# Performance work log

Hardware: AMD Instinct MI355X
Metric: run time of the kernel (lower is better)

The kernel has to match this reference:

```python
import jax, jax.numpy as jnp
import numpy as np

N_NODES, N_EDGES = 8000, 24000
MUL0_IN, MUL1_IN = 64, 32          # node: 64x0e + 32x1o
MUL0_MSG, MUL1_MSG = 16, 32        # msg:  16x0e + 32x1o
GATE_S, N_GATES = 16, 32           # gate scalars / gates (= mul of 32x1o gated)
RADIAL = 128
EDGE_DIM = 4                       # 1x0e + 1x1o
WNUM = MUL0_IN*MUL0_MSG + MUL0_IN*MUL1_MSG + MUL1_IN*MUL1_MSG + MUL1_IN*MUL0_MSG  # 4608
INV_SQRT3 = 1.0 / np.sqrt(3.0)     # wigner-3j(1,1,0)/(0,1,1)/(1,0,1) magnitude
# e3nn path weights: sqrt(ir_out.dim / sum_paths_into_output(num_elements))
PW_MSG0 = np.sqrt(1.0 / (MUL0_IN + MUL1_IN))                   # tp_msg -> 16x0e
PW_MSG1 = np.sqrt(3.0 / (MUL0_IN + MUL1_IN))                   # tp_msg -> 32x1o
PW_G01 = np.sqrt(1.0 / (MUL0_MSG*MUL0_IN + MUL1_MSG*MUL1_IN))  # FCTP -> 0e outs
PW_G2  = np.sqrt(3.0 / (MUL0_MSG*MUL1_IN + MUL1_MSG*MUL0_IN))  # FCTP -> 1o out
PW_H0 = np.sqrt(1.0 / (GATE_S + MUL1_MSG*MUL1_MSG))            # heavy_tp -> 16x0e
PW_H1 = np.sqrt(3.0 / (GATE_S + GATE_S))                       # heavy_tp -> 32x1o

_trapz = getattr(np, 'trapezoid', np.trapz)
def _cst(f):
    # e3nn normalize2mom constant: 1/sqrt(E_{z~N(0,1)}[f(z)^2])
    xs = np.linspace(-12.0, 12.0, 200001)
    pdf = np.exp(-0.5*xs*xs) / np.sqrt(2.0*np.pi)
    return float(1.0 / np.sqrt(_trapz(f(xs)**2 * pdf, xs)))
CST_SILU = _cst(lambda v: v / (1.0 + np.exp(-v)))
CST_SIG  = _cst(lambda v: 1.0 / (1.0 + np.exp(-v)))
CST_TANH = _cst(np.tanh)


def setup_inputs() -> dict:
    key = jax.random.key(0)
    ks = jax.random.split(key, 19)
    f = lambda k, s: jax.random.normal(k, s, dtype=jnp.float32)
    x = f(ks[0], (N_NODES, MUL0_IN + 3*MUL1_IN))
    edge_attr = f(ks[1], (N_EDGES, EDGE_DIM))
    edge_index = jax.random.randint(ks[2], (2, N_EDGES), 0, N_NODES)
    z = jax.random.randint(ks[3], (N_NODES,), 0, 10)
    canonical = jax.random.randint(ks[4], (N_NODES,), 0, N_NODES)
    W_mlp1 = f(ks[5], (EDGE_DIM, RADIAL))
    W_mlp2 = f(ks[6], (RADIAL, WNUM))
    Wg000 = f(ks[7], (MUL0_MSG, MUL0_IN, GATE_S))
    Wg110 = f(ks[8], (MUL1_MSG, MUL1_IN, GATE_S))
    Wg001 = f(ks[9], (MUL0_MSG, MUL0_IN, N_GATES))
    Wg111 = f(ks[10], (MUL1_MSG, MUL1_IN, N_GATES))
    Wg012 = f(ks[11], (MUL0_MSG, MUL1_IN, MUL1_MSG))
    Wg102 = f(ks[12], (MUL1_MSG, MUL0_IN, MUL1_MSG))
    Wa = f(ks[13], (GATE_S, GATE_S))
    Wb = f(ks[14], (GATE_S, MUL1_MSG))
    Wc = f(ks[15], (MUL1_MSG, GATE_S))
    Wd = f(ks[16], (MUL1_MSG, MUL1_MSG, GATE_S))
    WL0 = f(ks[17], (GATE_S, GATE_S))
    WL1 = f(ks[18], (MUL1_MSG, MUL1_MSG))
    return dict(x=x, edge_attr=edge_attr, W_mlp1=W_mlp1, W_mlp2=W_mlp2,
                Wg000=Wg000, Wg110=Wg110, Wg001=Wg001, Wg111=Wg111,
                Wg012=Wg012, Wg102=Wg102, Wa=Wa, Wb=Wb, Wc=Wc, Wd=Wd,
                WL0=WL0, WL1=WL1, edge_index=edge_index, z=z, canonical=canonical)


def _forward(x, edge_attr, W_mlp1, W_mlp2, Wg000, Wg110, Wg001, Wg111,
             Wg012, Wg102, Wa, Wb, Wc, Wd, WL0, WL1, edge_index, z, canonical):
    N = x.shape[0]
    E = edge_attr.shape[0]
    src, dst = edge_index[0], edge_index[1]
    # ---- radial MLP -> per-edge TP weights (e3nn FullyConnectedNet, normalized silu)
    h = CST_SILU * jax.nn.silu(edge_attr @ (W_mlp1 / np.sqrt(float(EDGE_DIM))))
    w = h @ (W_mlp2 / np.sqrt(float(RADIAL)))                 # (E, 4608)
    s000 = w[:, 0:1024].reshape(E, MUL0_IN, MUL0_MSG)
    s011 = w[:, 1024:3072].reshape(E, MUL0_IN, MUL1_MSG)
    s101 = w[:, 3072:4096].reshape(E, MUL1_IN, MUL1_MSG)
    s110 = w[:, 4096:4608].reshape(E, MUL1_IN, MUL0_MSG)
    # ---- gather source nodes, per-edge equivariant tensor product
    xs0 = x[src, :MUL0_IN]                                    # (E,64)
    xs1 = x[src, MUL0_IN:].reshape(E, MUL1_IN, 3)             # (E,32,3)
    a0 = edge_attr[:, 0]
    a1 = edge_attr[:, 1:4]
    msg0 = PW_MSG0 * (jnp.einsum('e,eu,euw->ew', a0, xs0, s000)
                      + INV_SQRT3 * jnp.einsum('eum,em,euw->ew', xs1, a1, s110))
    msg1 = PW_MSG1 * INV_SQRT3 * (jnp.einsum('eu,em,euw->ewm', xs0, a1, s011)
                                  + jnp.einsum('eum,e,euw->ewm', xs1, a0, s101))
    msg = jnp.concatenate([msg0, msg1.reshape(E, -1)], axis=-1)   # (E,112)
    # ---- scatter_add to destination nodes
    nm = jax.ops.segment_sum(msg, dst, num_segments=N)
    m0 = nm[:, :MUL0_MSG]
    m1 = nm[:, MUL0_MSG:].reshape(N, MUL1_MSG, 3)
    x0 = x[:, :MUL0_IN]
    x1 = x[:, MUL0_IN:].reshape(N, MUL1_IN, 3)
    # ---- FullyConnectedTensorProduct(msg, node) -> scalars | gates | gated
    gs = PW_G01 * (jnp.einsum('nu,nv,uvw->nw', m0, x0, Wg000)
                   + INV_SQRT3 * jnp.einsum('num,nvm,uvw->nw', m1, x1, Wg110))
    gg = PW_G01 * (jnp.einsum('nu,nv,uvw->nw', m0, x0, Wg001)
                   + INV_SQRT3 * jnp.einsum('num,nvm,uvw->nw', m1, x1, Wg111))
    gv = PW_G2 * INV_SQRT3 * (jnp.einsum('nu,nvm,uvw->nwm', m0, x1, Wg012)
                              + jnp.einsum('num,nv,uvw->nwm', m1, x0, Wg102))
    # ---- Gate (normalized sigmoid / tanh)
    xg0 = CST_SIG * jax.nn.sigmoid(gs)                        # (N,16)
    gates = CST_TANH * jnp.tanh(gg)                           # (N,32)
    xg1 = gates[:, :, None] * gv                              # (N,32,3)
    xg = jnp.concatenate([xg0, xg1.reshape(N, -1)], axis=-1)  # (N,112)
    # ---- heavy-atom pooling: scatter_mean of heavy nodes by canonical id
    mask = z > 1
    mf = mask.astype(x.dtype)
    sums = jax.ops.segment_sum(xg * mf[:, None], canonical, num_segments=N)
    cnt = jax.ops.segment_sum(mf, canonical, num_segments=N)
    xh = sums / jnp.maximum(cnt, 1.0)[:, None]
    h0 = xh[:, :GATE_S]
    h1 = xh[:, GATE_S:].reshape(N, MUL1_MSG, 3)
    # ---- heavy self tensor product (internal shared weights)
    t0 = PW_H0 * (jnp.einsum('uv,nu,nv->nu', Wa, h0, h0)
                  + INV_SQRT3 * jnp.einsum('uvw,num,nvm->nw', Wd, h1, h1))
    t1 = PW_H1 * INV_SQRT3 * (jnp.einsum('uv,nu,nvm->nvm', Wb, h0, h1)
                              + jnp.einsum('uv,num,nv->num', Wc, h1, h0))
    th = jnp.concatenate([t0, t1.reshape(N, -1)], axis=-1)
    # ---- broadcast heavy features back to heavy atoms
    y = jnp.where(mask[:, None], th[canonical], xg)
    y0 = y[:, :GATE_S]
    y1 = y[:, GATE_S:].reshape(N, MUL1_MSG, 3)
    # ---- e3nn Linear (per-irrep, 1/sqrt(fan_in))
    out0 = y0 @ (WL0 / np.sqrt(float(GATE_S)))
    out1 = jnp.einsum('num,uw->nwm', y1, WL1) / np.sqrt(float(MUL1_MSG))
    return jnp.concatenate([out0, out1.reshape(N, -1)], axis=-1)  # (N,112)


def reference(x, edge_attr, W_mlp1, W_mlp2, Wg000, Wg110, Wg001, Wg111,
              Wg012, Wg102, Wa, Wb, Wc, Wd, WL0, WL1, edge_index, z, canonical):
    return _forward(x, edge_attr, W_mlp1, W_mlp2, Wg000, Wg110, Wg001, Wg111,
                    Wg012, Wg102, Wa, Wb, Wc, Wd, WL0, WL1, edge_index, z, canonical)
```

## Files before the change

### kernel.cpp

```cpp
#include <hip/hip_runtime.h>
#include <hip/hip_bf16.h>
#include <cmath>


#define N_NODES 8000
#define N_EDGES 24000

#define INV_SQRT3f 0.57735026918962576f
#define PW_MSG0f 0.10206207261596575f
#define PW1f     0.10206207261596575f
#define PW_G01f  0.022097086912079608f
#define PW_G2f   0.034232659844072866f
#define PW_H0f   0.031008683647302115f
#define PW_H1f   0.30618621784789724f
#define RSQRT128f 0.08838834764831845f
#define RSQRT32f  0.17677669529663687f

typedef short short8 __attribute__((ext_vector_type(8)));
typedef short short4v __attribute__((ext_vector_type(4)));
typedef float f32x4 __attribute__((ext_vector_type(4)));

__device__ inline short f32_to_bf16_bits(float v) {
  unsigned int b = __builtin_bit_cast(unsigned int, v);
  b += 0x7fffu + ((b >> 16) & 1u);
  return (short)(b >> 16);
}

__global__ __launch_bounds__(256) void k1_h(const float* __restrict__ ea,
                                            const float* __restrict__ W1,
                                            short* __restrict__ hbf,
                                            float cst_silu) {
  int idx = blockIdx.x * 256 + threadIdx.x;
  int e = idx >> 5, q = idx & 31;
  const float a0 = ea[e*4+0], a1 = ea[e*4+1], a2 = ea[e*4+2], a3 = ea[e*4+3];
  const float4 w0 = *(const float4*)&W1[q*4];
  const float4 w1 = *(const float4*)&W1[128 + q*4];
  const float4 w2 = *(const float4*)&W1[256 + q*4];
  const float4 w3 = *(const float4*)&W1[384 + q*4];
  float s[4] = {0.5f*(a0*w0.x + a1*w1.x + a2*w2.x + a3*w3.x),
                0.5f*(a0*w0.y + a1*w1.y + a2*w2.y + a3*w3.y),
                0.5f*(a0*w0.z + a1*w1.z + a2*w2.z + a3*w3.z),
                0.5f*(a0*w0.w + a1*w1.w + a2*w2.w + a3*w3.w)};
  short4v o;
#pragma unroll
  for (int i = 0; i < 4; ++i) {
    float sg = 1.f / (1.f + expf(-s[i]));
    o[i] = f32_to_bf16_bits(cst_silu * s[i] * sg * RSQRT128f);
  }
  *(short4v*)&hbf[idx*4] = o;
}

__global__ __launch_bounds__(256) void k_prep(const float* __restrict__ W2,
                                              const float* __restrict__ Wg000,
                                              const float* __restrict__ Wg110,
                                              const float* __restrict__ Wg001,
                                              const float* __restrict__ Wg111,
                                              const float* __restrict__ Wg012,
                                              const float* __restrict__ Wg102,
                                              const float* __restrict__ Wd,
                                              const float* __restrict__ WL0,
                                              const float* __restrict__ WL1,
                                              short* __restrict__ w2s,
                                              short* __restrict__ bt,
                                              float* __restrict__ wdt,
                                              float* __restrict__ wl0t,
                                              float* __restrict__ wl1t) {
  const int b = blockIdx.x, tid = threadIdx.x;
  if (b < 576) {
    __shared__ float tile[32][33];
    const int kt = b & 3, ct = b >> 2;
    const int k0 = kt*32, c0 = ct*32;
    const int tx = tid & 31, ty = tid >> 5;
#pragma unroll
    for (int i = 0; i < 4; ++i) {
      int r = ty + i*8;
      tile[r][tx] = W2[(k0+r)*4608 + c0 + tx];
    }
    __syncthreads();
#pragma unroll
    for (int i = 0; i < 4; ++i) {
      int r = ty + i*8;
      const int c = c0 + r, k = k0 + tx;
      const int id = (c < 1024) ? (c >> 4)
                   : (c < 4096) ? ((c + 512) >> 4) : ((c - 3072) >> 4);
      const int nn = c & 15, ks = k >> 5, quad = (k >> 3) & 3, jj = k & 7;
      w2s[id*2048 + ks*512 + (quad*16 + nn)*8 + jj] = f32_to_bf16_bits(tile[tx][r]);
    }
  } else if (b < 1344) {
    int i = (b - 576) * 256 + tid;
    float v;
    if (i < 16384) {
      int u = i >> 10, r = i & 1023;
      int ks = r >> 9, lane = (r >> 3) & 63, j = r & 7;
      int k = ks*32 + (lane >> 4)*8 + j, nn = lane & 15;
      v = Wg000[u*1024 + k*16 + nn];
    } else if (i < 49152) {
      int o = i - 16384;
      int tau = o >> 10, r = o & 1023;
      int u = tau >> 1, wh = tau & 1;
      int ks = r >> 9, lane = (r >> 3) & 63, j = r & 7;
      int k = ks*32 + (lane >> 4)*8 + j, nn = lane & 15;
      v = Wg001[u*2048 + k*32 + wh*16 + nn];
    } else if (i < 65536) {
      int o = i - 49152;
      int u = o >> 9, r = o & 511;
      int lane = r >> 3, j = r & 7;
      int k = (lane >> 4)*8 + j, nn = lane & 15;
      v = INV_SQRT3f * Wg110[u*512 + k*16 + nn];
    } else if (i < 98304) {
      int o = i - 65536;
      int tau = o >> 9, r = o & 511;
      int u = tau >> 1, wh = tau & 1;
      int lane = r >> 3, j = r & 7;
      int k = (lane >> 4)*8 + j, nn = lane & 15;
      v = INV_SQRT3f * Wg111[u*1024 + k*32 + wh*16 + nn];
    } else if (i < 131072) {
      int o = i - 98304;
      int tau = o >> 9, r = o & 511;
      int vv = tau >> 1, wh = tau & 1;
      int lane = r >> 3, j = r & 7;
      int k = (lane >> 4)*8 + j, nn = lane & 15;
      v = (k < 16) ? Wg012[k*1024 + vv*32 + wh*16 + nn] : 0.f;
    } else {
      int o = i - 131072;
      int tau = o >> 10, r = o & 1023;
      int u = tau >> 1, wh = tau & 1;
      int ks = r >> 9, lane = (r >> 3) & 63, j = r & 7;
      int k = ks*32 + (lane >> 4)*8 + j, nn = lane & 15;
      v = Wg102[u*2048 + k*32 + wh*16 + nn];
    }
    bt[i] = f32_to_bf16_bits(v);
  } else {
    int i = (b - 1344) * 256 + tid;
    if (i < 16384) {
      int k = i >> 10, uv = i & 1023;
      wdt[i] = Wd[uv*16 + k];
    } else if (i < 16640) {
      int j = i - 16384; int jj = j >> 4, v = j & 15;
      wl0t[j] = WL0[v*16 + jj];
    } else if (i < 17664) {
      int j = i - 16640; int w = j >> 5, u = j & 31;
      wl1t[j] = WL1[u*32 + w];
    }
  }
}

__global__ __launch_bounds__(256, 2) void k2_edge_msg(
    const float* __restrict__ x, const float* __restrict__ ea,
    const short* __restrict__ w2s, const short* __restrict__ hbf,
    const int* __restrict__ ei, float* __restrict__ nm) {
  __shared__ float msg_s[32][116];
  __shared__ float x0pt[64][32];
  __shared__ float z2wt[32][32];
  __shared__ float x1wt[32][32][3];
  __shared__ float a_s[32][4];
  __shared__ int srcs_s[32], dsts_s[32];

  const int tid = threadIdx.x;
  const int e0 = blockIdx.x * 32;

  if (tid < 32) { srcs_s[tid] = ei[e0+tid]; dsts_s[tid] = ei[N_EDGES + e0 + tid]; }
  if (tid < 128) a_s[tid>>2][tid&3] = ea[e0*4 + tid];
  for (int i = tid; i < 32*116; i += 256) (&msg_s[0][0])[i] = 0.f;
  __syncthreads();

  for (int i = tid; i < 2048; i += 256) {
    int e = i >> 6, u = i & 63;
    x0pt[u][e] = PW1f * x[srcs_s[e]*160 + u];
  }
  for (int i = tid; i < 1024; i += 256) {
    int e = i >> 5, u = i & 31;
    const float* xp = &x[srcs_s[e]*160 + 64 + u*3];
    float m0v = xp[0], m1v = xp[1], m2v = xp[2];
    float a0 = a_s[e][0];
    z2wt[u][e] = PW_MSG0f * INV_SQRT3f *
                 (m0v*a_s[e][1] + m1v*a_s[e][2] + m2v*a_s[e][3]);
    x1wt[u][e][0] = PW1f * a0 * m0v;
    x1wt[u][e][1] = PW1f * a0 * m1v;
    x1wt[u][e][2] = PW1f * a0 * m2v;
  }
  __syncthreads();

  const int lane = tid & 63, wv = tid >> 6;
  const int quad = lane >> 4, nn = lane & 15;
  const int eq = quad * 4;

  short8 af[2][4];
#pragma unroll
  for (int t = 0; t < 2; ++t)
#pragma unroll
    for (int ks = 0; ks < 4; ++ks)
      af[t][ks] = *(const short8*)&hbf[(e0 + t*16 + nn)*128 + ks*32 + quad*8];

  float p000[2][4] = {};
  float p0[2][4] = {};
  float p011[2][4] = {};
  float p101[2][4][3] = {};

  short8 B0[4], B1[4], B2[4];
  auto loadB = [&](short8* B, int id) {
    const int idc = (id < 287) ? id : 287;
    const short* p = w2s + idc*2048 + lane*8;
    B[0] = *(const short8*)(p);
    B[1] = *(const short8*)(p + 512);
    B[2] = *(const short8*)(p + 1024);
    B[3] = *(const short8*)(p + 1536);
  };
  auto process = [&](const short8* B, int id) {
    f32x4 c0 = {0.f,0.f,0.f,0.f}, c1 = {0.f,0.f,0.f,0.f};
    c0 = __builtin_amdgcn_mfma_f32_16x16x32_bf16(af[0][0], B[0], c0, 0,0,0);
    c1 = __builtin_amdgcn_mfma_f32_16x16x32_bf16(af[1][0], B[0], c1, 0,0,0);
    c0 = __builtin_amdgcn_mfma_f32_16x16x32_bf16(af[0][1], B[1], c0, 0,0,0);
    c1 = __builtin_amdgcn_mfma_f32_16x16x32_bf16(af[1][1], B[1], c1, 0,0,0);
    c0 = __builtin_amdgcn_mfma_f32_16x16x32_bf16(af[0][2], B[2], c0, 0,0,0);
    c1 = __builtin_amdgcn_mfma_f32_16x16x32_bf16(af[1][2], B[2], c1, 0,0,0);
    c0 = __builtin_amdgcn_mfma_f32_16x16x32_bf16(af[0][3], B[3], c0, 0,0,0);
    c1 = __builtin_amdgcn_mfma_f32_16x16x32_bf16(af[1][3], B[3], c1, 0,0,0);
    if (id < 64) {
      const f32x4 w0 = *(const f32x4*)&x0pt[id][eq];
      const f32x4 w1 = *(const f32x4*)&x0pt[id][16 + eq];
#pragma unroll
      for (int r = 0; r < 4; ++r) { p000[0][r] += w0[r]*c0[r]; p000[1][r] += w1[r]*c1[r]; }
    } else if (id < 96) {
      const int u = id - 64;
      const f32x4 w0 = *(const f32x4*)&z2wt[u][eq];
      const f32x4 w1 = *(const f32x4*)&z2wt[u][16 + eq];
#pragma unroll
      for (int r = 0; r < 4; ++r) { p0[0][r] += w0[r]*c0[r]; p0[1][r] += w1[r]*c1[r]; }
    } else if (id < 224) {
      const int u = (id - 96) >> 1;
      const f32x4 w0 = *(const f32x4*)&x0pt[u][eq];
      const f32x4 w1 = *(const f32x4*)&x0pt[u][16 + eq];
#pragma unroll
      for (int r = 0; r < 4; ++r) { p011[0][r] += w0[r]*c0[r]; p011[1][r] += w1[r]*c1[r]; }
    } else {
      const int u = (id - 224) >> 1;
#pragma unroll
      for (int r = 0; r < 4; ++r) {
        const float* xw0 = &x1wt[u][eq + r][0];
        const float* xw1 = &x1wt[u][16 + eq + r][0];
        p101[0][r][0] += xw0[0]*c0[r]; p101[0][r][1] += xw0[1]*c0[r]; p101[0][r][2] += xw0[2]*c0[r];
        p101[1][r][0] += xw1[0]*c1[r]; p101[1][r][1] += xw1[1]*c1[r]; p101[1][r][2] += xw1[2]*c1[r];
      }
    }
  };

  loadB(B0, wv); loadB(B1, wv + 4);
  int id = wv;
  for (int j = 0; j < 24; ++j) {
    loadB(B2, id + 8);  __builtin_amdgcn_sched_barrier(0); process(B0, id);
    loadB(B0, id + 12); __builtin_amdgcn_sched_barrier(0); process(B1, id + 4);
    loadB(B1, id + 16); __builtin_amdgcn_sched_barrier(0); process(B2, id + 8);
    id += 12;
  }

  const int wcol = (wv & 1)*16 + nn;
#pragma unroll
  for (int t = 0; t < 2; ++t)
#pragma unroll
    for (int r = 0; r < 4; ++r) {
      const int e = t*16 + eq + r;
      atomicAdd(&msg_s[e][nn], a_s[e][0]*p000[t][r] + p0[t][r]);
      const float q = p011[t][r];
      atomicAdd(&msg_s[e][16 + wcol*3 + 0], a_s[e][1]*q + p101[t][r][0]);
      atomicAdd(&msg_s[e][16 + wcol*3 + 1], a_s[e][2]*q + p101[t][r][1]);
      atomicAdd(&msg_s[e][16 + wcol*3 + 2], a_s[e][3]*q + p101[t][r][2]);
    }
  __syncthreads();

  for (int i = tid; i < 32*112; i += 256) {
    int le = i / 112, slot = i - le*112;
    atomicAdd(&nm[dsts_s[le]*112 + slot], msg_s[le][slot]);
  }
}

__global__ __launch_bounds__(256, 2) void k3_gate(const float* __restrict__ x,
                                                  const float* __restrict__ nm,
                                                  const short* __restrict__ bt,
                                                  const int* __restrict__ z,
                                                  const int* __restrict__ canonical,
                                                  float* __restrict__ xg,
                                                  float* __restrict__ sums,
                                                  float* __restrict__ cnt,
                                                  float cst_sig, float cst_tanh) {
  __shared__ short x0b[16][64];
  __shared__ short x1b[3][16][32];
  __shared__ short m0b[16][32];
  __shared__ float m0t[16][16];
  __shared__ float m1t[32][3][16];
  __shared__ float x1t[32][3][16];
  __shared__ float gs_s[16][20];
  __shared__ float gg_s[16][36];
  __shared__ float gv_s[16][100];
  const int tid = threadIdx.x;
  const int n0 = blockIdx.x * 16;

  for (int i = tid; i < 16*160; i += 256) {
    int n = i / 160, f = i - n*160;
    float v = x[(n0+n)*160 + f];
    if (f < 64) x0b[n][f] = f32_to_bf16_bits(v);
    else {
      int j = f - 64; int vv = j/3, m = j - vv*3;
      x1b[m][n][vv] = f32_to_bf16_bits(v);
      x1t[vv][m][n] = v;
    }
  }
  for (int i = tid; i < 16*112; i += 256) {
    int n = i / 112, f = i - n*112;
    float v = nm[(n0+n)*112 + f];
    if (f < 16) { m0b[n][f] = f32_to_bf16_bits(v); m0t[f][n] = v; }
    else { int j = f - 16; int u = j/3, m = j - u*3; m1t[u][m][n] = v; }
  }
  { int n = tid >> 4, k = tid & 15; m0b[n][16+k] = 0; }
  for (int i = tid; i < 320; i += 256) (&gs_s[0][0])[i] = 0.f;
  for (int i = tid; i < 576; i += 256) (&gg_s[0][0])[i] = 0.f;
  for (int i = tid; i < 1600; i += 256) (&gv_s[0][0])[i] = 0.f;
  __syncthreads();

  const int lane = tid & 63, wv = tid >> 6;
  const int quad = lane >> 4, nn = lane & 15;
  const int eq = quad * 4;
  const int wh = wv & 1, uw = wv >> 1;
  const int l8 = lane * 8;

  const short8 ax0a = *(const short8*)&x0b[nn][quad*8];
  const short8 ax0c = *(const short8*)&x0b[nn][32 + quad*8];
  short8 ax1[3];
#pragma unroll
  for (int m = 0; m < 3; ++m) ax1[m] = *(const short8*)&x1b[m][nn][quad*8];
  const short8 am0 = *(const short8*)&m0b[nn][quad*8];

  const short* b000 = bt;
  const short* b001 = bt + 16384;
  const short* b110 = bt + 49152;
  const short* b111 = bt + 65536;
  const short* b012 = bt + 98304;
  const short* b102 = bt + 131072;

  float gs_p[4] = {}, gg_p[4] = {};
  float gv_p[3][4] = {};

  {
    int u = wv;
    const short* p = b000 + u*1024 + l8;
    short8 ba = *(const short8*)p, bb = *(const short8*)(p + 512);
    for (int i = 0; i < 4; ++i) {
      const int un = (i < 3) ? u + 4 : u;
      const short* np = b000 + un*1024 + l8;
      short8 na = *(const short8*)np, nb = *(const short8*)(np + 512);
      __builtin_amdgcn_sched_barrier(0);
      f32x4 c = {0.f,0.f,0.f,0.f};
      c = __builtin_amdgcn_mfma_f32_16x16x32_bf16(ax0a, ba, c, 0,0,0);
      c = __builtin_amdgcn_mfma_f32_16x16x32_bf16(ax0c, bb, c, 0,0,0);
      const f32x4 t = *(const f32x4*)&m0t[u][eq];
#pragma unroll
      for (int r = 0; r < 4; ++r) gs_p[r] += t[r]*c[r];
      u = un; ba = na; bb = nb;
    }
  }
  {
    int u = wv;
    short8 s0 = *(const short8*)(b110 + u*512 + l8);
    for (int i = 0; i < 8; ++i) {
      const int un = (i < 7) ? u + 4 : u;
      short8 ns = *(const short8*)(b110 + un*512 + l8);
      __builtin_amdgcn_sched_barrier(0);
      f32x4 c0 = {0.f,0.f,0.f,0.f}, c1 = {0.f,0.f,0.f,0.f}, c2 = {0.f,0.f,0.f,0.f};
      c0 = __builtin_amdgcn_mfma_f32_16x16x32_bf16(ax1[0], s0, c0, 0,0,0);
      c1 = __builtin_amdgcn_mfma_f32_16x16x32_bf16(ax1[1], s0, c1, 0,0,0);
      c2 = __builtin_amdgcn_mfma_f32_16x16x32_bf16(ax1[2], s0, c2, 0,0,0);
      const f32x4 t0 = *(const f32x4*)&m1t[u][0][eq];
      const f32x4 t1 = *(const f32x4*)&m1t[u][1][eq];
      const f32x4 t2 = *(const f32x4*)&m1t[u][2][eq];
#pragma unroll
      for (int r = 0; r < 4; ++r) gs_p[r] += t0[r]*c0[r] + t1[r]*c1[r] + t2[r]*c2[r];
      u = un; s0 = ns;
    }
  }
  {
    int u = uw;
    const short* p = b001 + (u*2 + wh)*1024 + l8;
    short8 ba = *(const short8*)p, bb = *(const short8*)(p + 512);
    for (int j = 0; j < 8; ++j) {
      const int un = (j < 7) ? u + 2 : u;
      const short* np = b001 + (un*2 + wh)*1024 + l8;
      short8 na = *(const short8*)np, nb = *(const short8*)(np + 512);
      __builtin_amdgcn_sched_barrier(0);
      f32x4 c = {0.f,0.f,0.f,0.f};
      c = __builtin_amdgcn_mfma_f32_16x16x32_bf16(ax0a, ba, c, 0,0,0);
      c = __builtin_amdgcn_mfma_f32_16x16x32_bf16(ax0c, bb, c, 0,0,0);
      const f32x4 t = *(const f32x4*)&m0t[u][eq];
#pragma unroll
      for (int r = 0; r < 4; ++r) gg_p[r] += t[r]*c[r];
      u = un; ba = na; bb = nb;
    }
  }
  {
    int u = uw;
    short8 s0 = *(const short8*)(b111 + (u*2 + wh)*512 + l8);
    for (int j = 0; j < 16; ++j) {
      const int un = (j < 15) ? u + 2 : u;
      short8 ns = *(const short8*)(b111 + (un*2 + wh)*512 + l8);
      __builtin_amdgcn_sched_barrier(0);
      f32x4 c0 = {0.f,0.f,0.f,0.f}, c1 = {0.f,0.f,0.f,0.f}, c2 = {0.f,0.f,0.f,0.f};
      c0 = __builtin_amdgcn_mfma_f32_16x16x32_bf16(ax1[0], s0, c0, 0,0,0);
      c1 = __builtin_amdgcn_mfma_f32_16x16x32_bf16(ax1[1], s0, c1, 0,0,0);
      c2 = __builtin_amdgcn_mfma_f32_16x16x32_bf16(ax1[2], s0, c2, 0,0,0);
      const f32x4 t0 = *(const f32x4*)&m1t[u][0][eq];
      const f32x4 t1 = *(const f32x4*)&m1t[u][1][eq];
      const f32x4 t2 = *(const f32x4*)&m1t[u][2][eq];
#pragma unroll
      for (int r = 0; r < 4; ++r) gg_p[r] += t0[r]*c0[r] + t1[r]*c1[r] + t2[r]*c2[r];
      u = un; s0 = ns;
    }
  }
  {
    int v = uw;
    short8 s0 = *(const short8*)(b012 + (v*2 + wh)*512 + l8);
    for (int j = 0; j < 16; ++j) {
      const int vn = (j < 15) ? v + 2 : v;
      short8 ns = *(const short8*)(b012 + (vn*2 + wh)*512 + l8);
      __builtin_amdgcn_sched_barrier(0);
      f32x4 c = {0.f,0.f,0.f,0.f};
      c = __builtin_amdgcn_mfma_f32_16x16x32_bf16(am0, s0, c, 0,0,0);
#pragma unroll
      for (int m = 0; m < 3; ++m) {
        const f32x4 t = *(const f32x4*)&x1t[v][m][eq];
#pragma unroll
        for (int r = 0; r < 4; ++r) gv_p[m][r] += t[r]*c[r];
      }
      v = vn; s0 = ns;
    }
  }
  {
    int u = uw;
    const short* p = b102 + (u*2 + wh)*1024 + l8;
    short8 ba = *(const short8*)p, bb = *(const short8*)(p + 512);
    for (int j = 0; j < 16; ++j) {
      const int un = (j < 15) ? u + 2 : u;
      const short* np = b102 + (un*2 + wh)*1024 + l8;
      short8 na = *(const short8*)np, nb = *(const short8*)(np + 512);
      __builtin_amdgcn_sched_barrier(0);
      f32x4 c = {0.f,0.f,0.f,0.f};
      c = __builtin_amdgcn_mfma_f32_16x16x32_bf16(ax0a, ba, c, 0,0,0);
      c = __builtin_amdgcn_mfma_f32_16x16x32_bf16(ax0c, bb, c, 0,0,0);
#pragma unroll
      for (int m = 0; m < 3; ++m) {
        const f32x4 t = *(const f32x4*)&m1t[u][m][eq];
#pragma unroll
        for (int r = 0; r < 4; ++r) gv_p[m][r] += t[r]*c[r];
      }
      u = un; ba = na; bb = nb;
    }
  }

#pragma unroll
  for (int r = 0; r < 4; ++r) {
    atomicAdd(&gs_s[eq + r][nn], gs_p[r]);
    atomicAdd(&gg_s[eq + r][wh*16 + nn], gg_p[r]);
#pragma unroll
    for (int m = 0; m < 3; ++m)
      atomicAdd(&gv_s[eq + r][(wh*16 + nn)*3 + m], gv_p[m][r]);
  }
  __syncthreads();

  for (int i = tid; i < 16*112; i += 256) {
    int n = i / 112, f = i - n*112;
    float o;
    if (f < 16) {
      o = cst_sig / (1.f + expf(-PW_G01f * gs_s[n][f]));
    } else {
      int j = f - 16; int w = j/3;
      float gate = cst_tanh * tanhf(PW_G01f * gg_s[n][w]);
      o = gate * (PW_G2f * INV_SQRT3f) * gv_s[n][j];
    }
    const int gn = n0 + n;
    xg[gn*112 + f] = o;
    if (z[gn] > 1) {
      const int c = canonical[gn];
      atomicAdd(&sums[c*112 + f], o);
      if (f == 0) atomicAdd(&cnt[c], 1.f);
    }
  }
}

__global__ __launch_bounds__(256) void k5_thead(const float* __restrict__ sums,
                                                const float* __restrict__ cnt,
                                                const float* __restrict__ Wa,
                                                const float* __restrict__ Wb,
                                                const float* __restrict__ Wc,
                                                const float* __restrict__ wdt,
                                                float* __restrict__ th) {
  __shared__ float xh_s[8][112];
  __shared__ float cm_s[8][1024];
  __shared__ float red[256];
  const int tid = threadIdx.x;
  const int n0 = blockIdx.x * 8;
  for (int i = tid; i < 8*112; i += 256) {
    int n = i / 112, j = i - n*112;
    float cv = fmaxf(cnt[n0+n], 1.f);
    xh_s[n][j] = sums[(n0+n)*112 + j] / cv;
  }
  __syncthreads();
  for (int i = tid; i < 8192; i += 256) {
    int n = i >> 10, uv = i & 1023, u = uv >> 5, v = uv & 31;
    const float* hh = xh_s[n] + 16;
    cm_s[n][uv] = hh[u*3]*hh[v*3] + hh[u*3+1]*hh[v*3+1] + hh[u*3+2]*hh[v*3+2];
  }
  __syncthreads();
  {
    const int hs = tid >> 7, p = tid & 127;
    const int n = p >> 4, k = p & 15;
    float wd = 0.f;
    const float* cp = cm_s[n] + hs*512;
    const float* wp = wdt + k*1024 + hs*512;
#pragma unroll 4
    for (int uv = 0; uv < 512; uv += 4) {
      const f32x4 a = *(const f32x4*)&cp[uv];
      const f32x4 bq = *(const f32x4*)&wp[uv];
      wd += a[0]*bq[0] + a[1]*bq[1] + a[2]*bq[2] + a[3]*bq[3];
    }
    red[tid] = wd;
  }
  __syncthreads();
  if (tid < 128) {
    int n = tid >> 4, k = tid & 15;
    float sA = 0.f;
    for (int v = 0; v < 16; ++v) sA += Wa[k*16+v]*xh_s[n][v];
    float wd = red[tid] + red[tid + 128];
    th[(n0+n)*112 + k] = PW_H0f*(xh_s[n][k]*sA + INV_SQRT3f*wd);
  }
  {
    int n = tid >> 5, j = tid & 31;
    float wb = 0.f, wc = 0.f;
    for (int u = 0; u < 16; ++u) wb += Wb[u*32+j]*xh_s[n][u];
    for (int v = 0; v < 16; ++v) wc += Wc[j*16+v]*xh_s[n][v];
    float cb = PW_H1f * INV_SQRT3f * (wb + wc);
    const float* hh = xh_s[n] + 16;
    float* o = th + (n0+n)*112 + 16 + j*3;
    o[0] = cb*hh[j*3]; o[1] = cb*hh[j*3+1]; o[2] = cb*hh[j*3+2];
  }
}

__global__ __launch_bounds__(256) void k6_out(const float* __restrict__ xg,
                                              const float* __restrict__ th,
                                              const int* __restrict__ z,
                                              const int* __restrict__ canonical,
                                              const float* __restrict__ wl0t,
                                              const float* __restrict__ wl1t,
                                              float* __restrict__ out) {
  int idx = blockIdx.x * 256 + threadIdx.x;
  int n = idx / 112, j = idx - n*112;
  const float* yr = (z[n] > 1) ? (th + canonical[n]*112) : (xg + n*112);
  float o = 0.f;
  if (j < 16) {
    const float* wp = wl0t + j*16;
#pragma unroll 4
    for (int v = 0; v < 16; ++v) o += yr[v]*wp[v];
    o *= 0.25f;
  } else {
    int jj = j - 16, w = jj / 3, m = jj - w*3;
    const float* wp = wl1t + w*32;
#pragma unroll 4
    for (int u = 0; u < 32; ++u) o += yr[16 + u*3 + m]*wp[u];
    o *= RSQRT32f;
  }
  out[idx] = o;
}

namespace {
struct Csts {
  float silu, sig, tanh_;
  Csts() {
    const int NPT = 200001;
    const double a = -12.0, b = 12.0;
    const double dx = (b - a) / (NPT - 1);
    double s1 = 0.0, s2 = 0.0, s3 = 0.0;
    for (int i = 0; i < NPT; ++i) {
      double xv = a + dx*i;
      double pdf = std::exp(-0.5*xv*xv) / std::sqrt(2.0*M_PI);
      double sg = 1.0 / (1.0 + std::exp(-xv));
      double f1 = xv*sg, f2 = sg, f3 = std::tanh(xv);
      double wg = (i == 0 || i == NPT-1) ? 0.5 : 1.0;
      s1 += wg*f1*f1*pdf; s2 += wg*f2*f2*pdf; s3 += wg*f3*f3*pdf;
    }
    silu  = (float)(1.0/std::sqrt(s1*dx));
    sig   = (float)(1.0/std::sqrt(s2*dx));
    tanh_ = (float)(1.0/std::sqrt(s3*dx));
  }
};
}

extern "C" void kernel_launch(void* const* d_in, const int* in_sizes, int n_in,
                              void* d_out, int out_size, void* d_ws, size_t ws_size,
                              hipStream_t stream) {
  const float* x     = (const float*)d_in[0];
  const float* ea    = (const float*)d_in[1];
  const float* W1    = (const float*)d_in[2];
  const float* W2    = (const float*)d_in[3];
  const float* Wg000 = (const float*)d_in[4];
  const float* Wg110 = (const float*)d_in[5];
  const float* Wg001 = (const float*)d_in[6];
  const float* Wg111 = (const float*)d_in[7];
  const float* Wg012 = (const float*)d_in[8];
  const float* Wg102 = (const float*)d_in[9];
  const float* Wa    = (const float*)d_in[10];
  const float* Wb    = (const float*)d_in[11];
  const float* Wc    = (const float*)d_in[12];
  const float* Wd    = (const float*)d_in[13];
  const float* WL0   = (const float*)d_in[14];
  const float* WL1   = (const float*)d_in[15];
  const int* ei      = (const int*)d_in[16];
  const int* z       = (const int*)d_in[17];
  const int* canonical = (const int*)d_in[18];
  float* out = (float*)d_out;

  float* ws   = (float*)d_ws;
  short* hbf  = (short*)ws;
  short* w2s  = (short*)(ws + 1536000);
  short* bt   = (short*)(ws + 1831000);
  float* nm   = ws + 1930000;
  float* xg   = ws + 2826000;
  float* sums = ws + 3722000;
  float* cnt  = ws + 4618000;
  float* th   = ws + 4626000;
  float* wdt  = ws + 5522000;
  float* wl0t = ws + 5538384;
  float* wl1t = ws + 5538640;

  static const Csts C;

  hipMemsetAsync(nm, 0, 896000*sizeof(float), stream);
  hipMemsetAsync(sums, 0, (896000+8000)*sizeof(float), stream);

  k1_h<<<3000, 256, 0, stream>>>(ea, W1, hbf, C.silu);
  k_prep<<<1413, 256, 0, stream>>>(W2, Wg000, Wg110, Wg001, Wg111, Wg012,
                                   Wg102, Wd, WL0, WL1, w2s, bt, wdt, wl0t, wl1t);
  k2_edge_msg<<<750, 256, 0, stream>>>(x, ea, w2s, hbf, ei, nm);
  k3_gate<<<500, 256, 0, stream>>>(x, nm, bt, z, canonical, xg, sums, cnt,
                                   C.sig, C.tanh_);
  k5_thead<<<1000, 256, 0, stream>>>(sums, cnt, Wa, Wb, Wc, wdt, th);
  k6_out<<<3500, 256, 0, stream>>>(xg, th, z, canonical, wl0t, wl1t, out);
}
```

Measured before the change: 288.4 us.

## Split edge-message weight columns across block pairs with 64-edge tiles; fuse prep kernels

The edge message kernel now processes 64 edges per block, and each pair of blocks splits the 288 radial-weight column groups in half. Each B fragment loaded from the expanded W2 is therefore reused across four MFMA row tiles instead of two, halving W2 reloads per edge. The cost is more accumulator registers, duplicated x gathers in both halves of a pair, and more global atomics. Separately, the radial MLP kernel is folded into the prep kernel as extra blocks, and the workspace is reordered so nm, sums and cnt are cleared with a single memset, saving a launch and a memset.

```diff
diff --git a/kernel.cpp b/kernel.cpp
--- a/kernel.cpp
+++ b/kernel.cpp
@@ -24,30 +24,6 @@
   unsigned int b = __builtin_bit_cast(unsigned int, v);
   b += 0x7fffu + ((b >> 16) & 1u);
   return (short)(b >> 16);
-}
-
-__global__ __launch_bounds__(256) void k1_h(const float* __restrict__ ea,
-                                            const float* __restrict__ W1,
-                                            short* __restrict__ hbf,
-                                            float cst_silu) {
-  int idx = blockIdx.x * 256 + threadIdx.x;
-  int e = idx >> 5, q = idx & 31;
-  const float a0 = ea[e*4+0], a1 = ea[e*4+1], a2 = ea[e*4+2], a3 = ea[e*4+3];
-  const float4 w0 = *(const float4*)&W1[q*4];
-  const float4 w1 = *(const float4*)&W1[128 + q*4];
-  const float4 w2 = *(const float4*)&W1[256 + q*4];
-  const float4 w3 = *(const float4*)&W1[384 + q*4];
-  float s[4] = {0.5f*(a0*w0.x + a1*w1.x + a2*w2.x + a3*w3.x),
-                0.5f*(a0*w0.y + a1*w1.y + a2*w2.y + a3*w3.y),
-                0.5f*(a0*w0.z + a1*w1.z + a2*w2.z + a3*w3.z),
-                0.5f*(a0*w0.w + a1*w1.w + a2*w2.w + a3*w3.w)};
-  short4v o;
-#pragma unroll
-  for (int i = 0; i < 4; ++i) {
-    float sg = 1.f / (1.f + expf(-s[i]));
-    o[i] = f32_to_bf16_bits(cst_silu * s[i] * sg * RSQRT128f);
-  }
-  *(short4v*)&hbf[idx*4] = o;
 }
 
 __global__ __launch_bounds__(256) void k_prep(const float* __restrict__ W2,
@@ -60,11 +36,15 @@
                                               const float* __restrict__ Wd,
                                               const float* __restrict__ WL0,
                                               const float* __restrict__ WL1,
+                                              const float* __restrict__ ea,
+                                              const float* __restrict__ W1,
                                               short* __restrict__ w2s,
                                               short* __restrict__ bt,
                                               float* __restrict__ wdt,
                                               float* __restrict__ wl0t,
-                                              float* __restrict__ wl1t) {
+                                              float* __restrict__ wl1t,
+                                              short* __restrict__ hbf,
+                                              float cst_silu) {
   const int b = blockIdx.x, tid = threadIdx.x;
   if (b < 576) {
     __shared__ float tile[32][33];
@@ -130,7 +110,7 @@
       v = Wg102[u*2048 + k*32 + wh*16 + nn];
     }
     bt[i] = f32_to_bf16_bits(v);
-  } else {
+  } else if (b < 1413) {
     int i = (b - 1344) * 256 + tid;
     if (i < 16384) {
       int k = i >> 10, uv = i & 1023;
@@ -142,60 +122,50 @@
       int j = i - 16640; int w = j >> 5, u = j & 31;
       wl1t[j] = WL1[u*32 + w];
     }
-  }
-}
-
-__global__ __launch_bounds__(256, 2) void k2_edge_msg(
-    const float* __restrict__ x, const float* __restrict__ ea,
+  } else {
+    int idx = (b - 1413) * 256 + tid;
+    int e = idx >> 5, q = idx & 31;
+    const float a0 = ea[e*4+0], a1 = ea[e*4+1], a2 = ea[e*4+2], a3 = ea[e*4+3];
+    const float4 w0 = *(const float4*)&W1[q*4];
+    const float4 w1 = *(const float4*)&W1[128 + q*4];
+    const float4 w2 = *(const float4*)&W1[256 + q*4];
+    const float4 w3 = *(const float4*)&W1[384 + q*4];
+    float s[4] = {0.5f*(a0*w0.x + a1*w1.x + a2*w2.x + a3*w3.x),
+                  0.5f*(a0*w0.y + a1*w1.y + a2*w2.y + a3*w3.y),
+                  0.5f*(a0*w0.z + a1*w1.z + a2*w2.z + a3*w3.z),
+                  0.5f*(a0*w0.w + a1*w1.w + a2*w2.w + a3*w3.w)};
+    short4v o;
+#pragma unroll
+    for (int i = 0; i < 4; ++i) {
+      float sg = 1.f / (1.f + expf(-s[i]));
+      o[i] = f32_to_bf16_bits(cst_silu * s[i] * sg * RSQRT128f);
+    }
+    *(short4v*)&hbf[idx*4] = o;
+  }
+}
+
+template<int HALF>
+__device__ __forceinline__ void k2_body(
     const short* __restrict__ w2s, const short* __restrict__ hbf,
-    const int* __restrict__ ei, float* __restrict__ nm) {
-  __shared__ float msg_s[32][116];
-  __shared__ float x0pt[64][32];
-  __shared__ float z2wt[32][32];
-  __shared__ float x1wt[32][32][3];
-  __shared__ float a_s[32][4];
-  __shared__ int srcs_s[32], dsts_s[32];
-
-  const int tid = threadIdx.x;
-  const int e0 = blockIdx.x * 32;
-
-  if (tid < 32) { srcs_s[tid] = ei[e0+tid]; dsts_s[tid] = ei[N_EDGES + e0 + tid]; }
-  if (tid < 128) a_s[tid>>2][tid&3] = ea[e0*4 + tid];
-  for (int i = tid; i < 32*116; i += 256) (&msg_s[0][0])[i] = 0.f;
-  __syncthreads();
-
-  for (int i = tid; i < 2048; i += 256) {
-    int e = i >> 6, u = i & 63;
-    x0pt[u][e] = PW1f * x[srcs_s[e]*160 + u];
-  }
-  for (int i = tid; i < 1024; i += 256) {
-    int e = i >> 5, u = i & 31;
-    const float* xp = &x[srcs_s[e]*160 + 64 + u*3];
-    float m0v = xp[0], m1v = xp[1], m2v = xp[2];
-    float a0 = a_s[e][0];
-    z2wt[u][e] = PW_MSG0f * INV_SQRT3f *
-                 (m0v*a_s[e][1] + m1v*a_s[e][2] + m2v*a_s[e][3]);
-    x1wt[u][e][0] = PW1f * a0 * m0v;
-    x1wt[u][e][1] = PW1f * a0 * m1v;
-    x1wt[u][e][2] = PW1f * a0 * m2v;
-  }
-  __syncthreads();
-
+    float* __restrict__ nm,
+    float (*msg_s)[116], float (*x0pt)[64], float* ovl,
+    float (*a_s)[4], const int* dsts_s, int e0, int tid) {
   const int lane = tid & 63, wv = tid >> 6;
   const int quad = lane >> 4, nn = lane & 15;
   const int eq = quad * 4;
-
-  short8 af[2][4];
-#pragma unroll
-  for (int t = 0; t < 2; ++t)
+  const int wh = wv & 1;
+
+  short8 af[4][4];
+#pragma unroll
+  for (int t = 0; t < 4; ++t)
 #pragma unroll
     for (int ks = 0; ks < 4; ++ks)
       af[t][ks] = *(const short8*)&hbf[(e0 + t*16 + nn)*128 + ks*32 + quad*8];
 
-  float p000[2][4] = {};
-  float p0[2][4] = {};
-  float p011[2][4] = {};
-  float p101[2][4][3] = {};
+  float p011[4][4] = {};
+  float p000[4][4] = {};
+  float p0[4][4] = {};
+  float p101[4][4][3] = {};
 
   short8 B0[4], B1[4], B2[4];
   auto loadB = [&](short8* B, int id) {
@@ -207,71 +177,152 @@
     B[3] = *(const short8*)(p + 1536);
   };
   auto process = [&](const short8* B, int id) {
-    f32x4 c0 = {0.f,0.f,0.f,0.f}, c1 = {0.f,0.f,0.f,0.f};
-    c0 = __builtin_amdgcn_mfma_f32_16x16x32_bf16(af[0][0], B[0], c0, 0,0,0);
-    c1 = __builtin_amdgcn_mfma_f32_16x16x32_bf16(af[1][0], B[0], c1, 0,0,0);
-    c0 = __builtin_amdgcn_mfma_f32_16x16x32_bf16(af[0][1], B[1], c0, 0,0,0);
-    c1 = __builtin_amdgcn_mfma_f32_16x16x32_bf16(af[1][1], B[1], c1, 0,0,0);
-    c0 = __builtin_amdgcn_mfma_f32_16x16x32_bf16(af[0][2], B[2], c0, 0,0,0);
-    c1 = __builtin_amdgcn_mfma_f32_16x16x32_bf16(af[1][2], B[2], c1, 0,0,0);
-    c0 = __builtin_amdgcn_mfma_f32_16x16x32_bf16(af[0][3], B[3], c0, 0,0,0);
-    c1 = __builtin_amdgcn_mfma_f32_16x16x32_bf16(af[1][3], B[3], c1, 0,0,0);
-    if (id < 64) {
-      const f32x4 w0 = *(const f32x4*)&x0pt[id][eq];
-      const f32x4 w1 = *(const f32x4*)&x0pt[id][16 + eq];
-#pragma unroll
-      for (int r = 0; r < 4; ++r) { p000[0][r] += w0[r]*c0[r]; p000[1][r] += w1[r]*c1[r]; }
-    } else if (id < 96) {
-      const int u = id - 64;
-      const f32x4 w0 = *(const f32x4*)&z2wt[u][eq];
-      const f32x4 w1 = *(const f32x4*)&z2wt[u][16 + eq];
-#pragma unroll
-      for (int r = 0; r < 4; ++r) { p0[0][r] += w0[r]*c0[r]; p0[1][r] += w1[r]*c1[r]; }
-    } else if (id < 224) {
-      const int u = (id - 96) >> 1;
-      const f32x4 w0 = *(const f32x4*)&x0pt[u][eq];
-      const f32x4 w1 = *(const f32x4*)&x0pt[u][16 + eq];
-#pragma unroll
-      for (int r = 0; r < 4; ++r) { p011[0][r] += w0[r]*c0[r]; p011[1][r] += w1[r]*c1[r]; }
+    f32x4 c[4];
+#pragma unroll
+    for (int mt = 0; mt < 4; ++mt) c[mt] = (f32x4){0.f,0.f,0.f,0.f};
+#pragma unroll
+    for (int ks = 0; ks < 4; ++ks) {
+#pragma unroll
+      for (int mt = 0; mt < 4; ++mt)
+        c[mt] = __builtin_amdgcn_mfma_f32_16x16x32_bf16(af[mt][ks], B[ks], c[mt], 0,0,0);
+    }
+    if (HALF == 0) {
+      if (id < 64) {
+#pragma unroll
+        for (int mt = 0; mt < 4; ++mt) {
+          const f32x4 w = *(const f32x4*)&x0pt[id][mt*16 + eq];
+#pragma unroll
+          for (int r = 0; r < 4; ++r) p000[mt][r] += w[r]*c[mt][r];
+        }
+      } else if (id < 96) {
+        const int u = id - 64;
+#pragma unroll
+        for (int mt = 0; mt < 4; ++mt) {
+          const f32x4 w = *(const f32x4*)&ovl[u*64 + mt*16 + eq];
+#pragma unroll
+          for (int r = 0; r < 4; ++r) p0[mt][r] += w[r]*c[mt][r];
+        }
+      } else {
+        const int u = (id - 96) >> 1;
+#pragma unroll
+        for (int mt = 0; mt < 4; ++mt) {
+          const f32x4 w = *(const f32x4*)&x0pt[u][mt*16 + eq];
+#pragma unroll
+          for (int r = 0; r < 4; ++r) p011[mt][r] += w[r]*c[mt][r];
+        }
+      }
     } else {
-      const int u = (id - 224) >> 1;
-#pragma unroll
-      for (int r = 0; r < 4; ++r) {
-        const float* xw0 = &x1wt[u][eq + r][0];
-        const float* xw1 = &x1wt[u][16 + eq + r][0];
-        p101[0][r][0] += xw0[0]*c0[r]; p101[0][r][1] += xw0[1]*c0[r]; p101[0][r][2] += xw0[2]*c0[r];
-        p101[1][r][0] += xw1[0]*c1[r]; p101[1][r][1] += xw1[1]*c1[r]; p101[1][r][2] += xw1[2]*c1[r];
+      if (id < 224) {
+        const int u = (id - 96) >> 1;
+#pragma unroll
+        for (int mt = 0; mt < 4; ++mt) {
+          const f32x4 w = *(const f32x4*)&x0pt[u][mt*16 + eq];
+#pragma unroll
+          for (int r = 0; r < 4; ++r) p011[mt][r] += w[r]*c[mt][r];
+        }
+      } else {
+        const int u = (id - 224) >> 1;
+#pragma unroll
+        for (int mt = 0; mt < 4; ++mt)
+#pragma unroll
+          for (int r = 0; r < 4; ++r) {
+            const float* xw = &ovl[(u*64 + mt*16 + eq + r)*3];
+            p101[mt][r][0] += xw[0]*c[mt][r];
+            p101[mt][r][1] += xw[1]*c[mt][r];
+            p101[mt][r][2] += xw[2]*c[mt][r];
+          }
       }
     }
   };
 
-  loadB(B0, wv); loadB(B1, wv + 4);
-  int id = wv;
-  for (int j = 0; j < 24; ++j) {
+  int id = HALF*144 + wv;
+  loadB(B0, id); loadB(B1, id + 4);
+  for (int j = 0; j < 12; ++j) {
     loadB(B2, id + 8);  __builtin_amdgcn_sched_barrier(0); process(B0, id);
     loadB(B0, id + 12); __builtin_amdgcn_sched_barrier(0); process(B1, id + 4);
     loadB(B1, id + 16); __builtin_amdgcn_sched_barrier(0); process(B2, id + 8);
     id += 12;
   }
 
-  const int wcol = (wv & 1)*16 + nn;
-#pragma unroll
-  for (int t = 0; t < 2; ++t)
+  const int wcol = wh*16 + nn;
+#pragma unroll
+  for (int mt = 0; mt < 4; ++mt)
 #pragma unroll
     for (int r = 0; r < 4; ++r) {
-      const int e = t*16 + eq + r;
-      atomicAdd(&msg_s[e][nn], a_s[e][0]*p000[t][r] + p0[t][r]);
-      const float q = p011[t][r];
-      atomicAdd(&msg_s[e][16 + wcol*3 + 0], a_s[e][1]*q + p101[t][r][0]);
-      atomicAdd(&msg_s[e][16 + wcol*3 + 1], a_s[e][2]*q + p101[t][r][1]);
-      atomicAdd(&msg_s[e][16 + wcol*3 + 2], a_s[e][3]*q + p101[t][r][2]);
-    }
-  __syncthreads();
-
-  for (int i = tid; i < 32*112; i += 256) {
-    int le = i / 112, slot = i - le*112;
-    atomicAdd(&nm[dsts_s[le]*112 + slot], msg_s[le][slot]);
-  }
+      const int e = mt*16 + eq + r;
+      const float q = p011[mt][r];
+      if (HALF == 0) {
+        atomicAdd(&msg_s[e][nn], a_s[e][0]*p000[mt][r] + p0[mt][r]);
+        atomicAdd(&msg_s[e][16 + wcol*3 + 0], a_s[e][1]*q);
+        atomicAdd(&msg_s[e][16 + wcol*3 + 1], a_s[e][2]*q);
+        atomicAdd(&msg_s[e][16 + wcol*3 + 2], a_s[e][3]*q);
+      } else {
+        atomicAdd(&msg_s[e][16 + wcol*3 + 0], a_s[e][1]*q + p101[mt][r][0]);
+        atomicAdd(&msg_s[e][16 + wcol*3 + 1], a_s[e][2]*q + p101[mt][r][1]);
+        atomicAdd(&msg_s[e][16 + wcol*3 + 2], a_s[e][3]*q + p101[mt][r][2]);
+      }
+    }
+  __syncthreads();
+
+  if (HALF == 0) {
+    for (int i = tid; i < 64*112; i += 256) {
+      int le = i / 112, slot = i - le*112;
+      atomicAdd(&nm[dsts_s[le]*112 + slot], msg_s[le][slot]);
+    }
+  } else {
+    for (int i = tid; i < 64*96; i += 256) {
+      int le = i / 96, slot = 16 + (i - le*96);
+      atomicAdd(&nm[dsts_s[le]*112 + slot], msg_s[le][slot]);
+    }
+  }
+}
+
+__global__ __launch_bounds__(256, 2) void k2_edge_msg(
+    const float* __restrict__ x, const float* __restrict__ ea,
+    const short* __restrict__ w2s, const short* __restrict__ hbf,
+    const int* __restrict__ ei, float* __restrict__ nm) {
+  __shared__ float msg_s[64][116];
+  __shared__ float x0pt[64][64];
+  __shared__ float ovl[6144];
+  __shared__ float a_s[64][4];
+  __shared__ int srcs_s[64], dsts_s[64];
+
+  const int tid = threadIdx.x;
+  const int blk = blockIdx.x;
+  const int g = blk >> 1, half = blk & 1;
+  const int e0 = g * 64;
+
+  if (tid < 64) { srcs_s[tid] = ei[e0+tid]; dsts_s[tid] = ei[N_EDGES + e0 + tid]; }
+  a_s[tid>>2][tid&3] = ea[e0*4 + tid];
+  for (int i = tid; i < 64*116; i += 256) (&msg_s[0][0])[i] = 0.f;
+  __syncthreads();
+
+  for (int i = tid; i < 4096; i += 256) {
+    int e = i >> 6, u = i & 63;
+    x0pt[u][e] = PW1f * x[srcs_s[e]*160 + u];
+  }
+  if (half == 0) {
+    for (int i = tid; i < 2048; i += 256) {
+      int e = i >> 5, u = i & 31;
+      const float* xp = &x[srcs_s[e]*160 + 64 + u*3];
+      ovl[u*64 + e] = PW_MSG0f * INV_SQRT3f *
+                      (xp[0]*a_s[e][1] + xp[1]*a_s[e][2] + xp[2]*a_s[e][3]);
+    }
+  } else {
+    for (int i = tid; i < 2048; i += 256) {
+      int e = i >> 5, u = i & 31;
+      const float* xp = &x[srcs_s[e]*160 + 64 + u*3];
+      float a0 = a_s[e][0];
+      float* o = &ovl[(u*64 + e)*3];
+      o[0] = PW1f * a0 * xp[0];
+      o[1] = PW1f * a0 * xp[1];
+      o[2] = PW1f * a0 * xp[2];
+    }
+  }
+  __syncthreads();
+
+  if (half == 0) k2_body<0>(w2s, hbf, nm, msg_s, x0pt, ovl, a_s, dsts_s, e0, tid);
+  else           k2_body<1>(w2s, hbf, nm, msg_s, x0pt, ovl, a_s, dsts_s, e0, tid);
 }
 
 __global__ __launch_bounds__(256, 2) void k3_gate(const float* __restrict__ x,
@@ -620,9 +671,9 @@
   short* w2s  = (short*)(ws + 1536000);
   short* bt   = (short*)(ws + 1831000);
   float* nm   = ws + 1930000;
-  float* xg   = ws + 2826000;
-  float* sums = ws + 3722000;
-  float* cnt  = ws + 4618000;
+  float* sums = ws + 2826000;
+  float* cnt  = ws + 3722000;
+  float* xg   = ws + 3730000;
   float* th   = ws + 4626000;
   float* wdt  = ws + 5522000;
   float* wl0t = ws + 5538384;
@@ -630,12 +681,11 @@
 
   static const Csts C;
 
-  hipMemsetAsync(nm, 0, 896000*sizeof(float), stream);
-  hipMemsetAsync(sums, 0, (896000+8000)*sizeof(float), stream);
-
-  k1_h<<<3000, 256, 0, stream>>>(ea, W1, hbf, C.silu);
-  k_prep<<<1413, 256, 0, stream>>>(W2, Wg000, Wg110, Wg001, Wg111, Wg012,
-                                   Wg102, Wd, WL0, WL1, w2s, bt, wdt, wl0t, wl1t);
+  hipMemsetAsync(nm, 0, 1800000*sizeof(float), stream);
+
+  k_prep<<<4413, 256, 0, stream>>>(W2, Wg000, Wg110, Wg001, Wg111, Wg012,
+                                   Wg102, Wd, WL0, WL1, ea, W1,
+                                   w2s, bt, wdt, wl0t, wl1t, hbf, C.silu);
   k2_edge_msg<<<750, 256, 0, stream>>>(x, ea, w2s, hbf, ei, nm);
   k3_gate<<<500, 256, 0, stream>>>(x, nm, bt, z, canonical, xg, sums, cnt,
                                    C.sig, C.tanh_);
```

After: 359.1 us. +24.5%, slower.
